# Performance work log

Hardware: AMD Instinct MI355X
Metric: run time of the kernel (lower is better)

Reference implementation:

```python
import jax, jax.numpy as jnp
import numpy as np

K = 7        # local attention window (kernel_size)
PAD = 3      # (K-1)//2, keeps spatial dims
GROUPS = 8   # attention heads


def _unfold(t, k, H, W):
    """t: [B,C,H+k-1,W+k-1] -> [B,C,H,W,k,k] sliding-window patches (stride 1).
    Matches torch .unfold(2,k,1).unfold(3,k,1): first k over height offsets,
    second k over width offsets."""
    cols = [t[:, :, i:i + H, j:j + W] for i in range(k) for j in range(k)]
    p = jnp.stack(cols, axis=-1)  # [B,C,H,W,k*k]
    return p.reshape(t.shape[0], t.shape[1], H, W, k, k)


def setup_inputs() -> dict:
    key = jax.random.key(0)
    ks = jax.random.split(key, 6)
    B, C, O, H, Wd = 4, 128, 128, 64, 64
    x = jax.random.normal(ks[0], (B, C, H, Wd), dtype=jnp.float32)
    # 1x1 conv weights, kaiming normal fan_out (fan_out = O for 1x1)
    scale = (2.0 / O) ** 0.5
    Wq = jax.random.normal(ks[1], (O, C), dtype=jnp.float32) * scale
    Wk = jax.random.normal(ks[2], (O, C), dtype=jnp.float32) * scale
    Wv = jax.random.normal(ks[3], (O, C), dtype=jnp.float32) * scale
    rel_h = jax.random.normal(ks[4], (O // 2, 1, 1, K, 1), dtype=jnp.float32)
    rel_w = jax.random.normal(ks[5], (O // 2, 1, 1, 1, K), dtype=jnp.float32)
    return {"x": x, "Wq": Wq, "Wk": Wk, "Wv": Wv, "rel_h": rel_h, "rel_w": rel_w}


def reference(x, Wq, Wk, Wv, rel_h, rel_w):
    B, C, H, W = x.shape
    O = Wq.shape[0]
    g = GROUPS
    # 1x1 convs (no bias)
    q = jnp.einsum('bchw,oc->bohw', x, Wq)                    # [B,O,H,W]
    xp = jnp.pad(x, ((0, 0), (0, 0), (PAD, PAD), (PAD, PAD)))
    k = jnp.einsum('bchw,oc->bohw', xp, Wk)                   # [B,O,Hp,Wp]
    v = jnp.einsum('bchw,oc->bohw', xp, Wv)
    kp = _unfold(k, K, H, W)                                  # [B,O,H,W,K,K]
    vp = _unfold(v, K, H, W)
    # relative position embeddings: height on first half of channels, width on second
    kh, kw = jnp.split(kp, 2, axis=1)
    kp = jnp.concatenate([kh + rel_h, kw + rel_w], axis=1)    # [B,O,H,W,K,K]
    kp = kp.reshape(B, g, O // g, H, W, K * K)
    vp = vp.reshape(B, g, O // g, H, W, K * K)
    qg = q.reshape(B, g, O // g, H, W, 1)
    scores = (qg * kp).sum(axis=2)                            # [B,g,H,W,K*K]
    attn = jax.nn.softmax(scores, axis=-1)
    out = jnp.einsum('bghwn,bgchwn->bgchw', attn, vp)         # [B,g,O/g,H,W]
    return out.reshape(B, O, H, W)
```

## Files before the change

### kernel.cpp

```cpp
#include <hip/hip_runtime.h>
#include <hip/hip_bf16.h>

#define B_   4
#define C_   128
#define H_   64
#define W_   64
#define HW_  4096
#define KW_  7
#define PAD_ 3
#define G_   8
#define CPG_ 16

#define CPAD 136

#define TS    16
#define HALO  22
#define NHP   (HALO*HALO)
#define LP    24

typedef _Float16 f16x8 __attribute__((ext_vector_type(8)));
typedef _Float16 f16x2 __attribute__((ext_vector_type(2)));
typedef _Float16 h2    __attribute__((ext_vector_type(2)));
typedef float    f32x4 __attribute__((ext_vector_type(4)));

static __device__ __forceinline__ unsigned short f2h(float f) {
    _Float16 h = (_Float16)f;
    union { _Float16 h; unsigned short u; } cv; cv.h = h;
    return cv.u;
}

#if defined(__has_builtin)
#if __has_builtin(__builtin_amdgcn_fdot2)
#define HAVE_FDOT2 1
#endif
#endif

__global__ __launch_bounds__(256) void proj_mfma(
    const float* __restrict__ x,
    const float* __restrict__ Wq,
    const float* __restrict__ Wk,
    const float* __restrict__ Wv,
    unsigned short* __restrict__ qkv16)
{
    const int ptile = blockIdx.x;
    const int b     = blockIdx.y;
    const int mz    = blockIdx.z;
    const int m     = mz >> 1;
    const int oh    = mz & 1;
    const float* Wm = (m == 0) ? Wq : ((m == 1) ? Wk : Wv);
    const float* xb = x + (size_t)b * C_ * HW_;
    unsigned short* y = qkv16 + ((size_t)(m * B_ + b)) * HW_ * C_;
    const int p0  = ptile * 64;
    const int tid = threadIdx.x;

    __shared__ unsigned short wls[64 * CPAD];
    __shared__ unsigned short xls[64 * CPAD];

    #pragma unroll
    for (int it = 0; it < 8; ++it) {
        const int idx = tid + it * 256;
        const int o   = idx >> 5;
        const int c4  = (idx & 31) * 4;
        const float4 w4 = *(const float4*)(Wm + (size_t)(oh * 64 + o) * C_ + c4);
        ushort4 hh;
        hh.x = f2h(w4.x); hh.y = f2h(w4.y); hh.z = f2h(w4.z); hh.w = f2h(w4.w);
        *(ushort4*)(&wls[o * CPAD + c4]) = hh;
    }
    #pragma unroll
    for (int it = 0; it < 2; ++it) {
        const int idx = tid + it * 256;
        const int pq  = (idx & 15) * 4;
        const int cq  = (idx >> 4) * 4;
        const float* xp = xb + (size_t)cq * HW_ + p0 + pq;
        const float4 r0 = *(const float4*)(xp);
        const float4 r1 = *(const float4*)(xp + HW_);
        const float4 r2 = *(const float4*)(xp + 2 * HW_);
        const float4 r3 = *(const float4*)(xp + 3 * HW_);
        ushort4 hh;
        hh.x = f2h(r0.x); hh.y = f2h(r1.x); hh.z = f2h(r2.x); hh.w = f2h(r3.x);
        *(ushort4*)(&xls[(pq + 0) * CPAD + cq]) = hh;
        hh.x = f2h(r0.y); hh.y = f2h(r1.y); hh.z = f2h(r2.y); hh.w = f2h(r3.y);
        *(ushort4*)(&xls[(pq + 1) * CPAD + cq]) = hh;
        hh.x = f2h(r0.z); hh.y = f2h(r1.z); hh.z = f2h(r2.z); hh.w = f2h(r3.z);
        *(ushort4*)(&xls[(pq + 2) * CPAD + cq]) = hh;
        hh.x = f2h(r0.w); hh.y = f2h(r1.w); hh.z = f2h(r2.w); hh.w = f2h(r3.w);
        *(ushort4*)(&xls[(pq + 3) * CPAD + cq]) = hh;
    }
    __syncthreads();

    const int wv   = tid >> 6;
    const int lane = tid & 63;
    const int row  = lane & 15;
    const int kq   = lane >> 4;

    f32x4 acc[4];
    #pragma unroll
    for (int ot = 0; ot < 4; ++ot)
        acc[ot] = (f32x4){0.f, 0.f, 0.f, 0.f};

    #pragma unroll
    for (int ks = 0; ks < 4; ++ks) {
        const int cb = ks * 32 + kq * 8;
        const f16x8 bfrag = *(const f16x8*)(&xls[(wv * 16 + row) * CPAD + cb]);
        #pragma unroll
        for (int ot = 0; ot < 4; ++ot) {
            const f16x8 afrag = *(const f16x8*)(&wls[(ot * 16 + row) * CPAD + cb]);
            acc[ot] = __builtin_amdgcn_mfma_f32_16x16x32_f16(afrag, bfrag, acc[ot], 0, 0, 0);
        }
    }

    const int p = p0 + wv * 16 + row;
    #pragma unroll
    for (int ot = 0; ot < 4; ++ot) {
        const int got = oh * 4 + ot;
        ushort4 hh;
        hh.x = f2h(acc[ot][0]); hh.y = f2h(acc[ot][1]);
        hh.z = f2h(acc[ot][2]); hh.w = f2h(acc[ot][3]);
        *(ushort4*)(y + ((size_t)got * HW_ + p) * CPG_ + kq * 4) = hh;
    }
}

__global__ __launch_bounds__(256) void attn_kernel(
    const unsigned short* __restrict__ qkv16,
    const float* __restrict__ rel_h,
    const float* __restrict__ rel_w,
    float* __restrict__ out)
{
    const int tile = blockIdx.x;
    const int g    = blockIdx.y;
    const int b    = blockIdx.z;
    const int h0   = (tile >> 2) * TS;
    const int w0   = (tile & 3) * TS;
    const int c0   = g * CPG_;

    __shared__ unsigned short kvls[2][NHP * LP];

    const size_t gplane = (size_t)HW_ * CPG_;
    const size_t mplane = (size_t)B_ * G_ * gplane;
    const unsigned short* qb = qkv16              + ((size_t)b * G_ + g) * gplane;
    const unsigned short* kb = qkv16 + mplane     + ((size_t)b * G_ + g) * gplane;
    const unsigned short* vb = qkv16 + 2 * mplane + ((size_t)b * G_ + g) * gplane;

    const int tid = threadIdx.x;
    const int pw  = tid & 15;
    const int ph  = tid >> 4;
    const int pix = (h0 + ph) * W_ + (w0 + pw);

    const f16x8 q0 = *(const f16x8*)(qb + (size_t)pix * CPG_);
    const f16x8 q1 = *(const f16x8*)(qb + (size_t)pix * CPG_ + 8);

    #pragma unroll
    for (int it = 0; it < 8; ++it) {
        const int idx = tid + it * 256;
        if (idx < 2 * NHP * 2) {
            const int arr  = (idx >= NHP * 2) ? 1 : 0;
            const int r    = idx - arr * NHP * 2;
            const int lp   = r >> 1;
            const int half = r & 1;
            const int hy   = h0 + lp / HALO - PAD_;
            const int hx   = w0 + lp % HALO - PAD_;
            f16x8 val = (f16x8)(_Float16)0.f;
            if ((unsigned)hy < (unsigned)H_ && (unsigned)hx < (unsigned)W_) {
                const unsigned short* src = (arr ? vb : kb)
                    + (size_t)(hy * W_ + hx) * CPG_ + half * 8;
                val = *(const f16x8*)src;
            }
            *(f16x8*)(&kvls[arr][lp * LP + half * 8]) = val;
        }
    }

    float qv[CPG_];
    #pragma unroll
    for (int c = 0; c < 8; ++c) { qv[c] = (float)q0[c]; qv[8 + c] = (float)q1[c]; }

    const bool useH = (g < 4);
    const float* rp = useH ? (rel_h + c0 * KW_) : (rel_w + (c0 - 64) * KW_);
    float rel[KW_];
    #pragma unroll
    for (int t = 0; t < KW_; ++t) {
        float r = 0.f;
        #pragma unroll
        for (int c = 0; c < CPG_; ++c) r += qv[c] * rp[c * KW_ + t];
        rel[t] = r;
    }

    __syncthreads();

    float s[KW_ * KW_];
    float smax = -1e30f;
    #pragma unroll
    for (int i = 0; i < KW_; ++i) {
        #pragma unroll
        for (int j = 0; j < KW_; ++j) {
            const unsigned short* kp = &kvls[0][((ph + i) * HALO + (pw + j)) * LP];
            const f16x8 k0 = *(const f16x8*)(kp);
            const f16x8 k1 = *(const f16x8*)(kp + 8);
            float sc = useH ? rel[i] : rel[j];
#ifdef HAVE_FDOT2
            #pragma unroll
            for (int t = 0; t < 4; ++t) {
                sc = __builtin_amdgcn_fdot2((h2){q0[2*t], q0[2*t+1]},
                                            (h2){k0[2*t], k0[2*t+1]}, sc, false);
                sc = __builtin_amdgcn_fdot2((h2){q1[2*t], q1[2*t+1]},
                                            (h2){k1[2*t], k1[2*t+1]}, sc, false);
            }
#else
            #pragma unroll
            for (int c = 0; c < 8; ++c)
                sc += qv[c] * (float)k0[c] + qv[8 + c] * (float)k1[c];
#endif
            s[i * KW_ + j] = sc;
            smax = fmaxf(smax, sc);
        }
    }

    float denom = 0.f;
    #pragma unroll
    for (int n = 0; n < KW_ * KW_; ++n) {
        s[n] = __expf(s[n] - smax);
        denom += s[n];
    }
    const float rdenom = 1.f / denom;

    f16x2 acch[8];
    #pragma unroll
    for (int c = 0; c < 8; ++c) acch[c] = (f16x2){(_Float16)0.f, (_Float16)0.f};

    #pragma unroll
    for (int i = 0; i < KW_; ++i) {
        #pragma unroll
        for (int j = 0; j < KW_; ++j) {
            const _Float16 ah = (_Float16)s[i * KW_ + j];
            const f16x2 av = {ah, ah};
            const unsigned short* vp = &kvls[1][((ph + i) * HALO + (pw + j)) * LP];
            const f16x8 v0 = *(const f16x8*)(vp);
            const f16x8 v1 = *(const f16x8*)(vp + 8);
            #pragma unroll
            for (int c = 0; c < 4; ++c) {
                const f16x2 p0v = {v0[2 * c], v0[2 * c + 1]};
                const f16x2 p1v = {v1[2 * c], v1[2 * c + 1]};
                acch[c]     += av * p0v;
                acch[4 + c] += av * p1v;
            }
        }
    }

    float* ob = out + ((size_t)b * C_ + c0) * HW_;
    #pragma unroll
    for (int c = 0; c < 8; ++c) {
        ob[(size_t)(2 * c)     * HW_ + pix] = (float)acch[c][0] * rdenom;
        ob[(size_t)(2 * c + 1) * HW_ + pix] = (float)acch[c][1] * rdenom;
    }
}

extern "C" void kernel_launch(void* const* d_in, const int* in_sizes, int n_in,
                              void* d_out, int out_size, void* d_ws, size_t ws_size,
                              hipStream_t stream) {
    const float* x     = (const float*)d_in[0];
    const float* Wq    = (const float*)d_in[1];
    const float* Wk    = (const float*)d_in[2];
    const float* Wv    = (const float*)d_in[3];
    const float* rel_h = (const float*)d_in[4];
    const float* rel_w = (const float*)d_in[5];
    unsigned short* ws = (unsigned short*)d_ws;
    float* out = (float*)d_out;

    dim3 gA(HW_ / 64, B_, 6);
    proj_mfma<<<gA, 256, 0, stream>>>(x, Wq, Wk, Wv, ws);

    dim3 gB(16, G_, B_);
    attn_kernel<<<gB, 256, 0, stream>>>(ws, rel_h, rel_w, out);
}
```

Measured before the change: 31.54 us.

## Split attention window across two threads per pixel with smaller tiles

```diff
diff --git a/kernel.cpp b/kernel.cpp
--- a/kernel.cpp
+++ b/kernel.cpp
@@ -13,9 +13,11 @@
 
 #define CPAD 136
 
-#define TS    16
-#define HALO  22
-#define NHP   (HALO*HALO)
+#define TSH   8
+#define TSW   16
+#define HLY   14
+#define HLX   22
+#define NHP2  (HLY*HLX)
 #define LP    24
 
 typedef _Float16 f16x8 __attribute__((ext_vector_type(8)));
@@ -120,6 +122,48 @@
     }
 }
 
+static __device__ __forceinline__ float score_pos(
+    const unsigned short* kls, const f16x8 q0, const f16x8 q1,
+    int ph, int pw, int i, int j, float base)
+{
+    const unsigned short* kp = &kls[((ph + i) * HLX + (pw + j)) * LP];
+    const f16x8 k0 = *(const f16x8*)(kp);
+    const f16x8 k1 = *(const f16x8*)(kp + 8);
+    float sc = base;
+#ifdef HAVE_FDOT2
+    #pragma unroll
+    for (int t = 0; t < 4; ++t) {
+        sc = __builtin_amdgcn_fdot2((h2){q0[2*t], q0[2*t+1]},
+                                    (h2){k0[2*t], k0[2*t+1]}, sc, false);
+        sc = __builtin_amdgcn_fdot2((h2){q1[2*t], q1[2*t+1]},
+                                    (h2){k1[2*t], k1[2*t+1]}, sc, false);
+    }
+#else
+    #pragma unroll
+    for (int c = 0; c < 8; ++c)
+        sc += (float)q0[c] * (float)k0[c] + (float)q1[c] * (float)k1[c];
+#endif
+    return sc;
+}
+
+static __device__ __forceinline__ void pv_pos(
+    const unsigned short* vls, int ph, int pw, int i, int j,
+    float a, f16x2* acch)
+{
+    const _Float16 ah = (_Float16)a;
+    const f16x2 av = {ah, ah};
+    const unsigned short* vp = &vls[((ph + i) * HLX + (pw + j)) * LP];
+    const f16x8 v0 = *(const f16x8*)(vp);
+    const f16x8 v1 = *(const f16x8*)(vp + 8);
+    #pragma unroll
+    for (int c = 0; c < 4; ++c) {
+        const f16x2 p0v = {v0[2 * c], v0[2 * c + 1]};
+        const f16x2 p1v = {v1[2 * c], v1[2 * c + 1]};
+        acch[c]     += av * p0v;
+        acch[4 + c] += av * p1v;
+    }
+}
+
 __global__ __launch_bounds__(256) void attn_kernel(
     const unsigned short* __restrict__ qkv16,
     const float* __restrict__ rel_h,
@@ -129,11 +173,12 @@
     const int tile = blockIdx.x;
     const int g    = blockIdx.y;
     const int b    = blockIdx.z;
-    const int h0   = (tile >> 2) * TS;
-    const int w0   = (tile & 3) * TS;
+    const int h0   = (tile >> 2) * TSH;
+    const int w0   = (tile & 3) * TSW;
     const int c0   = g * CPG_;
 
-    __shared__ unsigned short kvls[2][NHP * LP];
+    __shared__ unsigned short kvls[2][NHP2 * LP];
+    __shared__ unsigned comb[128][11];
 
     const size_t gplane = (size_t)HW_ * CPG_;
     const size_t mplane = (size_t)B_ * G_ * gplane;
@@ -142,23 +187,27 @@
     const unsigned short* vb = qkv16 + 2 * mplane + ((size_t)b * G_ + g) * gplane;
 
     const int tid = threadIdx.x;
-    const int pw  = tid & 15;
-    const int ph  = tid >> 4;
+    const int px  = tid & 127;
+    const int hw  = tid >> 7;
+    const int pw  = px & 15;
+    const int ph  = px >> 4;
     const int pix = (h0 + ph) * W_ + (w0 + pw);
 
     const f16x8 q0 = *(const f16x8*)(qb + (size_t)pix * CPG_);
     const f16x8 q1 = *(const f16x8*)(qb + (size_t)pix * CPG_ + 8);
 
     #pragma unroll
-    for (int it = 0; it < 8; ++it) {
+    for (int it = 0; it < 5; ++it) {
         const int idx = tid + it * 256;
-        if (idx < 2 * NHP * 2) {
-            const int arr  = (idx >= NHP * 2) ? 1 : 0;
-            const int r    = idx - arr * NHP * 2;
+        if (idx < 2 * NHP2 * 2) {
+            const int arr  = (idx >= NHP2 * 2) ? 1 : 0;
+            const int r    = idx - arr * NHP2 * 2;
             const int lp   = r >> 1;
             const int half = r & 1;
-            const int hy   = h0 + lp / HALO - PAD_;
-            const int hx   = w0 + lp % HALO - PAD_;
+            const int yy   = lp / HLX;
+            const int ww   = lp - yy * HLX;
+            const int hy   = h0 + yy - PAD_;
+            const int hx   = w0 + ww - PAD_;
             f16x8 val = (f16x8)(_Float16)0.f;
             if ((unsigned)hy < (unsigned)H_ && (unsigned)hx < (unsigned)W_) {
                 const unsigned short* src = (arr ? vb : kb)
@@ -169,87 +218,97 @@
         }
     }
 
-    float qv[CPG_];
-    #pragma unroll
-    for (int c = 0; c < 8; ++c) { qv[c] = (float)q0[c]; qv[8 + c] = (float)q1[c]; }
-
     const bool useH = (g < 4);
     const float* rp = useH ? (rel_h + c0 * KW_) : (rel_w + (c0 - 64) * KW_);
     float rel[KW_];
-    #pragma unroll
-    for (int t = 0; t < KW_; ++t) {
-        float r = 0.f;
-        #pragma unroll
-        for (int c = 0; c < CPG_; ++c) r += qv[c] * rp[c * KW_ + t];
-        rel[t] = r;
+    {
+        float qv[CPG_];
+        #pragma unroll
+        for (int c = 0; c < 8; ++c) { qv[c] = (float)q0[c]; qv[8 + c] = (float)q1[c]; }
+        #pragma unroll
+        for (int t = 0; t < KW_; ++t) {
+            float r = 0.f;
+            #pragma unroll
+            for (int c = 0; c < CPG_; ++c) r += qv[c] * rp[c * KW_ + t];
+            rel[t] = r;
+        }
     }
 
     __syncthreads();
 
-    float s[KW_ * KW_];
-    float smax = -1e30f;
-    #pragma unroll
-    for (int i = 0; i < KW_; ++i) {
-        #pragma unroll
-        for (int j = 0; j < KW_; ++j) {
-            const unsigned short* kp = &kvls[0][((ph + i) * HALO + (pw + j)) * LP];
-            const f16x8 k0 = *(const f16x8*)(kp);
-            const f16x8 k1 = *(const f16x8*)(kp + 8);
-            float sc = useH ? rel[i] : rel[j];
-#ifdef HAVE_FDOT2
-            #pragma unroll
-            for (int t = 0; t < 4; ++t) {
-                sc = __builtin_amdgcn_fdot2((h2){q0[2*t], q0[2*t+1]},
-                                            (h2){k0[2*t], k0[2*t+1]}, sc, false);
-                sc = __builtin_amdgcn_fdot2((h2){q1[2*t], q1[2*t+1]},
-                                            (h2){k1[2*t], k1[2*t+1]}, sc, false);
-            }
-#else
-            #pragma unroll
-            for (int c = 0; c < 8; ++c)
-                sc += qv[c] * (float)k0[c] + qv[8 + c] * (float)k1[c];
-#endif
-            s[i * KW_ + j] = sc;
-            smax = fmaxf(smax, sc);
-        }
-    }
-
-    float denom = 0.f;
-    #pragma unroll
-    for (int n = 0; n < KW_ * KW_; ++n) {
-        s[n] = __expf(s[n] - smax);
-        denom += s[n];
-    }
-    const float rdenom = 1.f / denom;
-
+    const unsigned short* kls = kvls[0];
+    const unsigned short* vls = kvls[1];
+
+    float mloc, den = 0.f;
     f16x2 acch[8];
     #pragma unroll
     for (int c = 0; c < 8; ++c) acch[c] = (f16x2){(_Float16)0.f, (_Float16)0.f};
 
-    #pragma unroll
-    for (int i = 0; i < KW_; ++i) {
-        #pragma unroll
-        for (int j = 0; j < KW_; ++j) {
-            const _Float16 ah = (_Float16)s[i * KW_ + j];
-            const f16x2 av = {ah, ah};
-            const unsigned short* vp = &kvls[1][((ph + i) * HALO + (pw + j)) * LP];
-            const f16x8 v0 = *(const f16x8*)(vp);
-            const f16x8 v1 = *(const f16x8*)(vp + 8);
-            #pragma unroll
-            for (int c = 0; c < 4; ++c) {
-                const f16x2 p0v = {v0[2 * c], v0[2 * c + 1]};
-                const f16x2 p1v = {v1[2 * c], v1[2 * c + 1]};
-                acch[c]     += av * p0v;
-                acch[4 + c] += av * p1v;
-            }
-        }
-    }
-
-    float* ob = out + ((size_t)b * C_ + c0) * HW_;
-    #pragma unroll
-    for (int c = 0; c < 8; ++c) {
-        ob[(size_t)(2 * c)     * HW_ + pix] = (float)acch[c][0] * rdenom;
-        ob[(size_t)(2 * c + 1) * HW_ + pix] = (float)acch[c][1] * rdenom;
+    if (hw == 0) {
+        float s[25];
+        float m = -1e30f;
+        #pragma unroll
+        for (int r = 0; r < 25; ++r) {
+            const int n = 2 * r, i = n / 7, j = n % 7;
+            s[r] = score_pos(kls, q0, q1, ph, pw, i, j, useH ? rel[i] : rel[j]);
+            m = fmaxf(m, s[r]);
+        }
+        #pragma unroll
+        for (int r = 0; r < 25; ++r) { s[r] = __expf(s[r] - m); den += s[r]; }
+        #pragma unroll
+        for (int r = 0; r < 25; ++r) {
+            const int n = 2 * r, i = n / 7, j = n % 7;
+            pv_pos(vls, ph, pw, i, j, s[r], acch);
+        }
+        mloc = m;
+    } else {
+        float s[24];
+        float m = -1e30f;
+        #pragma unroll
+        for (int r = 0; r < 24; ++r) {
+            const int n = 2 * r + 1, i = n / 7, j = n % 7;
+            s[r] = score_pos(kls, q0, q1, ph, pw, i, j, useH ? rel[i] : rel[j]);
+            m = fmaxf(m, s[r]);
+        }
+        #pragma unroll
+        for (int r = 0; r < 24; ++r) { s[r] = __expf(s[r] - m); den += s[r]; }
+        #pragma unroll
+        for (int r = 0; r < 24; ++r) {
+            const int n = 2 * r + 1, i = n / 7, j = n % 7;
+            pv_pos(vls, ph, pw, i, j, s[r], acch);
+        }
+        mloc = m;
+    }
+
+    if (hw == 1) {
+        comb[px][0] = __float_as_uint(mloc);
+        comb[px][1] = __float_as_uint(den);
+        #pragma unroll
+        for (int c = 0; c < 8; ++c) {
+            union { f16x2 v; unsigned u; } cv; cv.v = acch[c];
+            comb[px][2 + c] = cv.u;
+        }
+    }
+    __syncthreads();
+
+    if (hw == 0) {
+        const float m1   = __uint_as_float(comb[px][0]);
+        const float den1 = __uint_as_float(comb[px][1]);
+        const float mC = fmaxf(mloc, m1);
+        const float f0 = __expf(mloc - mC);
+        const float f1 = __expf(m1 - mC);
+        const float rden = 1.f / (den * f0 + den1 * f1);
+
+        float* ob = out + ((size_t)b * C_ + c0) * HW_;
+        #pragma unroll
+        for (int c = 0; c < 8; ++c) {
+            union { unsigned u; f16x2 v; } cv; cv.u = comb[px][2 + c];
+            const f16x2 a1 = cv.v;
+            ob[(size_t)(2 * c)     * HW_ + pix] =
+                ((float)acch[c][0] * f0 + (float)a1[0] * f1) * rden;
+            ob[(size_t)(2 * c + 1) * HW_ + pix] =
+                ((float)acch[c][1] * f0 + (float)a1[1] * f1) * rden;
+        }
     }
 }
 
@@ -268,6 +327,6 @@
     dim3 gA(HW_ / 64, B_, 6);
     proj_mfma<<<gA, 256, 0, stream>>>(x, Wq, Wk, Wv, ws);
 
-    dim3 gB(16, G_, B_);
+    dim3 gB(32, G_, B_);
     attn_kernel<<<gB, 256, 0, stream>>>(ws, rel_h, rel_w, out);
 }
```

New measurement: 31.53 us. About the same (-0.1%).

## Compute Q, K, V projections in one block reusing the x tile

Applied to the files above, without the earlier changes.

```diff
diff --git a/kernel.cpp b/kernel.cpp
--- a/kernel.cpp
+++ b/kernel.cpp
@@ -44,28 +44,16 @@
 {
     const int ptile = blockIdx.x;
     const int b     = blockIdx.y;
-    const int mz    = blockIdx.z;
-    const int m     = mz >> 1;
-    const int oh    = mz & 1;
-    const float* Wm = (m == 0) ? Wq : ((m == 1) ? Wk : Wv);
+    const int oh    = blockIdx.z;
     const float* xb = x + (size_t)b * C_ * HW_;
-    unsigned short* y = qkv16 + ((size_t)(m * B_ + b)) * HW_ * C_;
     const int p0  = ptile * 64;
     const int tid = threadIdx.x;
 
-    __shared__ unsigned short wls[64 * CPAD];
+    const float* Wms[3] = {Wq, Wk, Wv};
+
+    __shared__ unsigned short wls[2][64 * CPAD];
     __shared__ unsigned short xls[64 * CPAD];
 
-    #pragma unroll
-    for (int it = 0; it < 8; ++it) {
-        const int idx = tid + it * 256;
-        const int o   = idx >> 5;
-        const int c4  = (idx & 31) * 4;
-        const float4 w4 = *(const float4*)(Wm + (size_t)(oh * 64 + o) * C_ + c4);
-        ushort4 hh;
-        hh.x = f2h(w4.x); hh.y = f2h(w4.y); hh.z = f2h(w4.z); hh.w = f2h(w4.w);
-        *(ushort4*)(&wls[o * CPAD + c4]) = hh;
-    }
     #pragma unroll
     for (int it = 0; it < 2; ++it) {
         const int idx = tid + it * 256;
@@ -86,37 +74,70 @@
         hh.x = f2h(r0.w); hh.y = f2h(r1.w); hh.z = f2h(r2.w); hh.w = f2h(r3.w);
         *(ushort4*)(&xls[(pq + 3) * CPAD + cq]) = hh;
     }
+
+    #pragma unroll
+    for (int it = 0; it < 8; ++it) {
+        const int idx = tid + it * 256;
+        const int o   = idx >> 5;
+        const int c4  = (idx & 31) * 4;
+        const float4 w4 = *(const float4*)(Wq + (size_t)(oh * 64 + o) * C_ + c4);
+        ushort4 hh;
+        hh.x = f2h(w4.x); hh.y = f2h(w4.y); hh.z = f2h(w4.z); hh.w = f2h(w4.w);
+        *(ushort4*)(&wls[0][o * CPAD + c4]) = hh;
+    }
     __syncthreads();
 
     const int wv   = tid >> 6;
     const int lane = tid & 63;
     const int row  = lane & 15;
     const int kq   = lane >> 4;
-
-    f32x4 acc[4];
-    #pragma unroll
-    for (int ot = 0; ot < 4; ++ot)
-        acc[ot] = (f32x4){0.f, 0.f, 0.f, 0.f};
-
-    #pragma unroll
-    for (int ks = 0; ks < 4; ++ks) {
-        const int cb = ks * 32 + kq * 8;
-        const f16x8 bfrag = *(const f16x8*)(&xls[(wv * 16 + row) * CPAD + cb]);
+    const int p    = p0 + wv * 16 + row;
+
+    #pragma unroll
+    for (int m = 0; m < 3; ++m) {
+        if (m < 2) {
+            const float* Wn = Wms[m + 1];
+            unsigned short* dst = wls[(m + 1) & 1];
+            #pragma unroll
+            for (int it = 0; it < 8; ++it) {
+                const int idx = tid + it * 256;
+                const int o   = idx >> 5;
+                const int c4  = (idx & 31) * 4;
+                const float4 w4 = *(const float4*)(Wn + (size_t)(oh * 64 + o) * C_ + c4);
+                ushort4 hh;
+                hh.x = f2h(w4.x); hh.y = f2h(w4.y); hh.z = f2h(w4.z); hh.w = f2h(w4.w);
+                *(ushort4*)(&dst[o * CPAD + c4]) = hh;
+            }
+        }
+
+        const unsigned short* wcur = wls[m & 1];
+        f32x4 acc[4];
+        #pragma unroll
+        for (int ot = 0; ot < 4; ++ot)
+            acc[ot] = (f32x4){0.f, 0.f, 0.f, 0.f};
+
+        #pragma unroll
+        for (int ks = 0; ks < 4; ++ks) {
+            const int cb = ks * 32 + kq * 8;
+            const f16x8 bfrag = *(const f16x8*)(&xls[(wv * 16 + row) * CPAD + cb]);
+            #pragma unroll
+            for (int ot = 0; ot < 4; ++ot) {
+                const f16x8 afrag = *(const f16x8*)(&wcur[(ot * 16 + row) * CPAD + cb]);
+                acc[ot] = __builtin_amdgcn_mfma_f32_16x16x32_f16(afrag, bfrag, acc[ot], 0, 0, 0);
+            }
+        }
+
+        unsigned short* y = qkv16 + ((size_t)(m * B_ + b)) * HW_ * C_;
         #pragma unroll
         for (int ot = 0; ot < 4; ++ot) {
-            const f16x8 afrag = *(const f16x8*)(&wls[(ot * 16 + row) * CPAD + cb]);
-            acc[ot] = __builtin_amdgcn_mfma_f32_16x16x32_f16(afrag, bfrag, acc[ot], 0, 0, 0);
-        }
-    }
-
-    const int p = p0 + wv * 16 + row;
-    #pragma unroll
-    for (int ot = 0; ot < 4; ++ot) {
-        const int got = oh * 4 + ot;
-        ushort4 hh;
-        hh.x = f2h(acc[ot][0]); hh.y = f2h(acc[ot][1]);
-        hh.z = f2h(acc[ot][2]); hh.w = f2h(acc[ot][3]);
-        *(ushort4*)(y + ((size_t)got * HW_ + p) * CPG_ + kq * 4) = hh;
+            const int got = oh * 4 + ot;
+            ushort4 hh;
+            hh.x = f2h(acc[ot][0]); hh.y = f2h(acc[ot][1]);
+            hh.z = f2h(acc[ot][2]); hh.w = f2h(acc[ot][3]);
+            *(ushort4*)(y + ((size_t)got * HW_ + p) * CPG_ + kq * 4) = hh;
+        }
+
+        if (m < 2) __syncthreads();
     }
 }
 
@@ -265,7 +286,7 @@
     unsigned short* ws = (unsigned short*)d_ws;
     float* out = (float*)d_out;
 
-    dim3 gA(HW_ / 64, B_, 6);
+    dim3 gA(HW_ / 64, B_, 2);
     proj_mfma<<<gA, 256, 0, stream>>>(x, Wq, Wk, Wv, ws);
 
     dim3 gB(16, G_, B_);
```

New measurement: 31.52 us. Within noise of the previous version (-0.1%).
